# Kernel tuning notes

Measured on AMD Instinct MI355X. Metric: run time of the kernel, lower is better.

The kernel has to match this reference:

```python
import jax, jax.numpy as jnp
import numpy as np

B, N, D = 64, 100, 32            # batch, nodes, node feature size
FE = [96, 160, 192]              # edge-MLP layer sizes
FN = [256, 256, 32]              # node-MLP layer sizes
ALPHA = 0.2                      # leaky relu slope


def _lin_init(key, fan_in, fan_out):
    kw, kb = jax.random.split(key)
    bound = 1.0 / np.sqrt(fan_in)
    w = jax.random.uniform(kw, (fan_in, fan_out), jnp.float32, -bound, bound)
    b = jax.random.uniform(kb, (fan_out,), jnp.float32, -bound, bound)
    return w, b


def setup_inputs() -> dict:
    key = jax.random.key(0)
    ks = jax.random.split(key, 7)
    d = {"x": jax.random.normal(ks[0], (B, N, D), jnp.float32)}
    fe_sizes = [2 * D] + FE                    # edge MLP: in = concat(x_i, x_j)
    fn_sizes = [FE[-1] + D] + FN               # node MLP: in = concat(agg, x)
    for li in range(3):
        w, b = _lin_init(ks[1 + li], fe_sizes[li], fe_sizes[li + 1])
        d[f"fe_w{li}"], d[f"fe_b{li}"] = w, b
    for li in range(3):
        w, b = _lin_init(ks[4 + li], fn_sizes[li], fn_sizes[li + 1])
        d[f"fn_w{li}"], d[f"fn_b{li}"] = w, b
    return d


def reference(x, fe_w0, fe_b0, fe_w1, fe_b1, fe_w2, fe_b2,
              fn_w0, fn_b0, fn_w1, fn_b1, fn_w2, fn_b2):
    b, n, d = x.shape
    lr = lambda v: jax.nn.leaky_relu(v, ALPHA)
    # fully-connected pairwise edge features: A[b,i,j] = concat(x_i, x_j)
    xi = jnp.broadcast_to(x[:, :, None, :], (b, n, n, d))
    xj = jnp.broadcast_to(x[:, None, :, :], (b, n, n, d))
    a = jnp.concatenate([xi, xj], axis=-1)          # [b, n, n, 2d]
    # edge MLP (fe): leaky relu after every layer (final_linear=False)
    a = lr(a @ fe_w0 + fe_b0)
    a = lr(a @ fe_w1 + fe_b1)
    a = lr(a @ fe_w2 + fe_b2)                       # [b, n, n, FE[-1]]
    # sum aggregation over neighbors j
    agg = jnp.sum(a, axis=2)                        # [b, n, FE[-1]]
    # node MLP (fn): final layer linear (final_linear=True)
    h = jnp.concatenate([agg, x], axis=-1)          # [b, n, FE[-1]+d]
    h = lr(h @ fn_w0 + fn_b0)
    h = lr(h @ fn_w1 + fn_b1)
    h = h @ fn_w2 + fn_b2                           # [b, n, FN[-1]]
    return h
```

## Files before the change

kernel.cpp:

```cpp
#include <hip/hip_runtime.h>

#define B_    64
#define N_    100
#define D_    32
#define F0    96
#define F1    160
#define F2    192
#define HID   256
#define FOUT  32

typedef unsigned short u16;
typedef unsigned int   u32;
typedef u16   u16x8 __attribute__((ext_vector_type(8)));
typedef u32   u32x2 __attribute__((ext_vector_type(2)));
typedef __bf16 bf16x8 __attribute__((ext_vector_type(8)));
typedef float  fx4   __attribute__((ext_vector_type(4)));

__device__ __forceinline__ u16 f2bf(float f) {
    return __builtin_bit_cast(u16, (__bf16)f);
}
__device__ __forceinline__ float lrelu(float v) { return fmaxf(v, 0.2f * v); }

__device__ __forceinline__ bf16x8 fragLds(const u16* p) {
    return __builtin_bit_cast(bf16x8, *(const u16x8*)p);
}
__device__ __forceinline__ bf16x8 fragGbl(const u16* __restrict__ p) {
    return __builtin_bit_cast(bf16x8, *(const u16x8*)p);
}
#define MFMA(a, b, c) __builtin_amdgcn_mfma_f32_16x16x32_bf16((a), (b), (c), 0, 0, 0)

__device__ __forceinline__ u32x2 quadPack(u32 h) {
    u32 h1 = (u32)__shfl_xor((int)h, 1, 64);
    u32 pk = h | (h1 << 16);
    u32 pko = (u32)__shfl_xor((int)pk, 2, 64);
    return (u32x2){pk, pko};
}

#define OFF_P     0u
#define OFF_V     2457600u
#define OFF_AGG   4915200u
#define OFF_PACK  7372800u
#define PK_W1     0
#define PK_W2     15360
#define PK_N0     46080
#define PK_N1     103424
#define PK_N2     168960
#define PK_TOTAL  177152

#define PV_BLOCKS 2400
#define PACK_BLOCKS 346

__global__ __launch_bounds__(512) void prep_kernel(
    const float* __restrict__ x,
    const float* __restrict__ few0, const float* __restrict__ feb0,
    const float* __restrict__ few1, const float* __restrict__ few2,
    const float* __restrict__ fnw0, const float* __restrict__ fnw1,
    const float* __restrict__ fnw2,
    float* __restrict__ P, float* __restrict__ V, u16* __restrict__ wpack)
{
    const int blk = blockIdx.x, tid = threadIdx.x;
    if (blk < PV_BLOCKS) {
        int o = blk * 512 + tid;
        int r = o / 192, h = o - r * 192;
        const float* xr = x + r * D_;
        if (h < F0) {
            float acc = feb0[h];
            #pragma unroll
            for (int d = 0; d < D_; ++d) acc = fmaf(xr[d], few0[d * F0 + h], acc);
            P[r * F0 + h] = acc;
        } else {
            int k = h - F0;
            float acc = 0.f;
            #pragma unroll
            for (int d = 0; d < D_; ++d) acc = fmaf(xr[d], few0[(D_ + d) * F0 + k], acc);
            V[r * F0 + k] = acc;
        }
    } else {
        int p = (blk - PV_BLOCKS) * 512 + tid;
        const float* src; int start, Ncols, NT;
        if (p < PK_W2)      { start = PK_W1; src = few1; Ncols = F1;   NT = 10; }
        else if (p < PK_N0) { start = PK_W2; src = few2; Ncols = F2;   NT = 12; }
        else if (p < PK_N1) { start = PK_N0; src = fnw0; Ncols = HID;  NT = 16; }
        else if (p < PK_N2) { start = PK_N1; src = fnw1; Ncols = HID;  NT = 16; }
        else                { start = PK_N2; src = fnw2; Ncols = FOUT; NT = 2;  }
        int local = p - start;
        int j = local & 7, lane = (local >> 3) & 63, rest = local >> 9;
        int nt = rest % NT, kt = rest / NT;
        int n = 16 * nt + (lane & 15);
        int k = 32 * kt + 8 * (lane >> 4) + j;
        wpack[p] = f2bf(src[k * Ncols + n]);
    }
}

__global__ __launch_bounds__(512, 4) void edge_kernel(
    const float* __restrict__ P, const float* __restrict__ V,
    const u16* __restrict__ W1p, const u16* __restrict__ W2p,
    const float* __restrict__ feb1, const float* __restrict__ feb2,
    u16* __restrict__ agg)
{
    const int i = blockIdx.x, b = blockIdx.y;
    const int tid = threadIdx.x, ld = tid & 63, wv = tid >> 6;
    const int wn = wv & 3, wm = wv >> 2;
    const int row = b * N_ + i;

    __shared__ __align__(16) u16  sA0p[7 * 3 * 512];
    __shared__ __align__(16) u16  sA1p[7 * 5 * 512];
    __shared__ __align__(16) float sP[F0];
    __shared__ __align__(16) float sAggP[2 * F2];

    if (tid < F0) sP[tid] = P[row * F0 + tid];
    __syncthreads();

    {
        const float* Vb = V + b * N_ * F0;
        #pragma unroll
        for (int s = 0; s < 3; ++s) {
            int idx = tid + 512 * s;
            if (idx < 1344) {
                int lane = idx & 63, rest = idx >> 6;
                int kt = rest % 3, mt = rest / 3;
                int k = 32 * kt + 8 * (lane >> 4);
                int m = 16 * mt + (lane & 15);
                u16x8 w;
                if (m < N_) {
                    const float* vp = Vb + m * F0 + k;
                    fx4 v0 = *(const fx4*)(vp);
                    fx4 v1 = *(const fx4*)(vp + 4);
                    fx4 p0 = *(const fx4*)(sP + k);
                    fx4 p1 = *(const fx4*)(sP + k + 4);
                    #pragma unroll
                    for (int jj = 0; jj < 4; ++jj) {
                        w[jj]     = f2bf(lrelu(p0[jj] + v0[jj]));
                        w[4 + jj] = f2bf(lrelu(p1[jj] + v1[jj]));
                    }
                } else {
                    w = (u16x8){0, 0, 0, 0, 0, 0, 0, 0};
                }
                *(u16x8*)(sA0p + idx * 8) = w;
            }
        }
    }
    __syncthreads();

    const int mtB = wm ? 4 : 0, mtE = wm ? 7 : 4;
    const int c = ld & 15, rlo = (ld >> 4) * 4;
    const int a1off = (ld * 16) ^ (((ld >> 3) & 7) << 4);

    {
        const int nCnt = (wn < 2) ? 3 : 2;
        bf16x8 bw[3][3]; float bias[3];
        #pragma unroll
        for (int t = 0; t < 3; ++t) if (t < nCnt) {
            int nt = wn + 4 * t;
            bias[t] = feb1[16 * nt + c];
            #pragma unroll
            for (int kt = 0; kt < 3; ++kt)
                bw[t][kt] = fragGbl(W1p + (size_t)((kt * 10 + nt) * 64 + ld) * 8);
        }
        for (int mt = mtB; mt < mtE; ++mt) {
            bf16x8 a[3];
            #pragma unroll
            for (int kt = 0; kt < 3; ++kt)
                a[kt] = fragLds(sA0p + ((mt * 3 + kt) * 64 + ld) * 8);
            fx4 acc[3];
            #pragma unroll
            for (int t = 0; t < 3; ++t) acc[t] = (fx4){0.f, 0.f, 0.f, 0.f};
            #pragma unroll
            for (int kt = 0; kt < 3; ++kt)
                #pragma unroll
                for (int t = 0; t < 3; ++t)
                    if (t < nCnt) acc[t] = MFMA(a[kt], bw[t][kt], acc[t]);
            #pragma unroll
            for (int t = 0; t < 3; ++t) if (t < nCnt) {
                int nt = wn + 4 * t;
                int f = 16 * nt + c;
                int lq = (f >> 3) & 3;
                int S  = (((rlo >> 3) + 2 * lq) & 7) << 4;
                char* base = (char*)sA1p + (mt * 5 + (nt >> 1)) * 1024 + (c & 4) * 2;
                #pragma unroll
                for (int r = 0; r < 4; ++r) {
                    u32 h = (u32)f2bf(lrelu(acc[t][r] + bias[t]));
                    u32x2 two = quadPack(h);
                    int rowl = rlo + 16 * lq + r;
                    if ((ld & 3) == 0)
                        *(u32x2*)(base + ((rowl * 16) ^ S)) = two;
                }
            }
        }
    }
    __syncthreads();

    {
        bf16x8 bw[3][5]; float bias[3];
        float aggp[3] = {0.f, 0.f, 0.f};
        #pragma unroll
        for (int t = 0; t < 3; ++t) {
            int nt = wn + 4 * t;
            bias[t] = feb2[16 * nt + c];
            #pragma unroll
            for (int kt = 0; kt < 5; ++kt)
                bw[t][kt] = fragGbl(W2p + (size_t)((kt * 12 + nt) * 64 + ld) * 8);
        }
        for (int mt = mtB; mt < mtE; ++mt) {
            bf16x8 a[5];
            const char* rb = (const char*)sA1p + mt * 5120 + a1off;
            #pragma unroll
            for (int kt = 0; kt < 5; ++kt)
                a[kt] = fragLds((const u16*)(rb + kt * 1024));
            fx4 acc[3];
            #pragma unroll
            for (int t = 0; t < 3; ++t) acc[t] = (fx4){0.f, 0.f, 0.f, 0.f};
            #pragma unroll
            for (int kt = 0; kt < 5; ++kt)
                #pragma unroll
                for (int t = 0; t < 3; ++t)
                    acc[t] = MFMA(a[kt], bw[t][kt], acc[t]);
            bool ok = (mt < 6) || (rlo == 0);
            if (ok) {
                #pragma unroll
                for (int t = 0; t < 3; ++t)
                    #pragma unroll
                    for (int r = 0; r < 4; ++r)
                        aggp[t] += lrelu(acc[t][r] + bias[t]);
            }
        }
        #pragma unroll
        for (int t = 0; t < 3; ++t) {
            aggp[t] += __shfl_xor(aggp[t], 16, 64);
            aggp[t] += __shfl_xor(aggp[t], 32, 64);
        }
        if (ld < 16) {
            #pragma unroll
            for (int t = 0; t < 3; ++t)
                sAggP[wm * F2 + 16 * (wn + 4 * t) + ld] = aggp[t];
        }
    }
    __syncthreads();

    if (tid < F2) {
        float v = sAggP[tid] + sAggP[F2 + tid];
        agg[(size_t)row * F2 + tid] = f2bf(v);
    }
}

__global__ __launch_bounds__(512, 4) void node_kernel(
    const u16* __restrict__ agg, const float* __restrict__ x,
    const u16* __restrict__ n0p, const u16* __restrict__ n1p,
    const u16* __restrict__ n2p,
    const float* __restrict__ fnb0, const float* __restrict__ fnb1,
    const float* __restrict__ fnb2,
    float* __restrict__ out)
{
    const int blk = blockIdx.x;
    const int tid = threadIdx.x, ld = tid & 63, wv = tid >> 6;
    const int wn = wv & 3, mt = wv >> 2;
    const int c = ld & 15, rlo = (ld >> 4) * 4;
    const int c0 = c & ~3;

    __shared__ __align__(16) u16 sH0p[2 * 7 * 512];
    __shared__ __align__(16) u16 sH1p[2 * 8 * 512];
    __shared__ __align__(16) u16 sH2p[2 * 8 * 512];

    #pragma unroll
    for (int s = 0; s < 2; ++s) {
        int idx = tid + 512 * s;
        if (idx < 896) {
            int lane = idx & 63, rest = idx >> 6;
            int kt = rest % 7, mtt = rest / 7;
            int k = 32 * kt + 8 * (lane >> 4);
            int m = 16 * mtt + (lane & 15);
            int g = 32 * blk + m;
            u16x8 w;
            if (k < F2) {
                w = *(const u16x8*)(agg + (size_t)g * F2 + k);
            } else {
                const float* xp = x + (size_t)g * D_ + (k - F2);
                fx4 v0 = *(const fx4*)xp;
                fx4 v1 = *(const fx4*)(xp + 4);
                #pragma unroll
                for (int jj = 0; jj < 4; ++jj) {
                    w[jj] = f2bf(v0[jj]); w[4 + jj] = f2bf(v1[jj]);
                }
            }
            *(u16x8*)(sH0p + idx * 8) = w;
        }
    }
    __syncthreads();

    {
        fx4 acc[4];
        #pragma unroll
        for (int t = 0; t < 4; ++t) acc[t] = (fx4){0.f, 0.f, 0.f, 0.f};
        for (int kt = 0; kt < 7; ++kt) {
            bf16x8 a = fragLds(sH0p + ((mt * 7 + kt) * 64 + ld) * 8);
            #pragma unroll
            for (int t = 0; t < 4; ++t) {
                bf16x8 bw = fragGbl(n0p + (size_t)((kt * 16 + wn + 4 * t) * 64 + ld) * 8);
                acc[t] = MFMA(a, bw, acc[t]);
            }
        }
        #pragma unroll
        for (int t = 0; t < 4; ++t) {
            int f = 16 * (wn + 4 * t) + c;
            float bias = fnb0[f];
            int kt2 = f >> 5, lq = (f >> 3) & 3;
            u16* basep = sH1p + ((mt * 8 + kt2) * 64 + rlo + 16 * lq) * 8 + (c0 & 7);
            #pragma unroll
            for (int r = 0; r < 4; ++r) {
                u32 h = (u32)f2bf(lrelu(acc[t][r] + bias));
                u32x2 two = quadPack(h);
                if ((ld & 3) == 0)
                    *(u32x2*)(basep + r * 8) = two;
            }
        }
    }
    __syncthreads();

    {
        fx4 acc[4];
        #pragma unroll
        for (int t = 0; t < 4; ++t) acc[t] = (fx4){0.f, 0.f, 0.f, 0.f};
        for (int kt = 0; kt < 8; ++kt) {
            bf16x8 a = fragLds(sH1p + ((mt * 8 + kt) * 64 + ld) * 8);
            #pragma unroll
            for (int t = 0; t < 4; ++t) {
                bf16x8 bw = fragGbl(n1p + (size_t)((kt * 16 + wn + 4 * t) * 64 + ld) * 8);
                acc[t] = MFMA(a, bw, acc[t]);
            }
        }
        #pragma unroll
        for (int t = 0; t < 4; ++t) {
            int f = 16 * (wn + 4 * t) + c;
            float bias = fnb1[f];
            int kt2 = f >> 5, lq = (f >> 3) & 3;
            u16* basep = sH2p + ((mt * 8 + kt2) * 64 + rlo + 16 * lq) * 8 + (c0 & 7);
            #pragma unroll
            for (int r = 0; r < 4; ++r) {
                u32 h = (u32)f2bf(lrelu(acc[t][r] + bias));
                u32x2 two = quadPack(h);
                if ((ld & 3) == 0)
                    *(u32x2*)(basep + r * 8) = two;
            }
        }
    }
    __syncthreads();

    if (wv < 4) {
        int mt2 = wv >> 1, nt = wv & 1;
        fx4 acc = (fx4){0.f, 0.f, 0.f, 0.f};
        for (int kt = 0; kt < 8; ++kt) {
            bf16x8 a = fragLds(sH2p + ((mt2 * 8 + kt) * 64 + ld) * 8);
            bf16x8 bw = fragGbl(n2p + (size_t)((kt * 2 + nt) * 64 + ld) * 8);
            acc = MFMA(a, bw, acc);
        }
        int f = 16 * nt + c;
        float bias = fnb2[f];
        #pragma unroll
        for (int r = 0; r < 4; ++r) {
            int g = 32 * blk + 16 * mt2 + rlo + r;
            out[(size_t)g * FOUT + f] = acc[r] + bias;
        }
    }
}

extern "C" void kernel_launch(void* const* d_in, const int* in_sizes, int n_in,
                              void* d_out, int out_size, void* d_ws, size_t ws_size,
                              hipStream_t stream) {
    const float* x    = (const float*)d_in[0];
    const float* few0 = (const float*)d_in[1];
    const float* feb0 = (const float*)d_in[2];
    const float* few1 = (const float*)d_in[3];
    const float* feb1 = (const float*)d_in[4];
    const float* few2 = (const float*)d_in[5];
    const float* feb2 = (const float*)d_in[6];
    const float* fnw0 = (const float*)d_in[7];
    const float* fnb0 = (const float*)d_in[8];
    const float* fnw1 = (const float*)d_in[9];
    const float* fnb1 = (const float*)d_in[10];
    const float* fnw2 = (const float*)d_in[11];
    const float* fnb2 = (const float*)d_in[12];

    char* w = (char*)d_ws;
    float* P    = (float*)(w + OFF_P);
    float* V    = (float*)(w + OFF_V);
    u16*   aggb = (u16*)(w + OFF_AGG);
    u16*   pack = (u16*)(w + OFF_PACK);

    prep_kernel<<<PV_BLOCKS + PACK_BLOCKS, 512, 0, stream>>>(
        x, few0, feb0, few1, few2, fnw0, fnw1, fnw2, P, V, pack);

    edge_kernel<<<dim3(N_, B_), 512, 0, stream>>>(
        P, V, pack + PK_W1, pack + PK_W2, feb1, feb2, aggb);

    node_kernel<<<200, 512, 0, stream>>>(
        aggb, x, pack + PK_N0, pack + PK_N1, pack + PK_N2,
        fnb0, fnb1, fnb2, (float*)d_out);
}
```

Measured before the change: 245.8 us.

## Split edge kernel neighbor range across two blocks with atomic fp32 aggregation

Each (row, batch) edge block is split along the neighbor dimension into two blocks via a z grid dimension, each handling about half of the 7 neighbor tiles with smaller shared-memory buffers. Partial sums are combined with fp32 atomicAdd into a float aggregate buffer, which prep_kernel zeroes, and node_kernel converts to bf16 when loading. The aim is more parallelism and lower per-block LDS use, which should raise occupancy. In exchange the work per block is uneven (4 vs 3 tiles), the P/V setup and weight-fragment loads are repeated in both halves, and the atomics and larger fp32 intermediate add memory traffic.

```diff
diff --git a/kernel.cpp b/kernel.cpp
--- a/kernel.cpp
+++ b/kernel.cpp
@@ -39,7 +39,7 @@
 #define OFF_P     0u
 #define OFF_V     2457600u
 #define OFF_AGG   4915200u
-#define OFF_PACK  7372800u
+#define OFF_PACK  9830400u
 #define PK_W1     0
 #define PK_W2     15360
 #define PK_N0     46080
@@ -56,11 +56,13 @@
     const float* __restrict__ few1, const float* __restrict__ few2,
     const float* __restrict__ fnw0, const float* __restrict__ fnw1,
     const float* __restrict__ fnw2,
-    float* __restrict__ P, float* __restrict__ V, u16* __restrict__ wpack)
+    float* __restrict__ P, float* __restrict__ V, u16* __restrict__ wpack,
+    float* __restrict__ aggF)
 {
     const int blk = blockIdx.x, tid = threadIdx.x;
     if (blk < PV_BLOCKS) {
         int o = blk * 512 + tid;
+        aggF[o] = 0.f;
         int r = o / 192, h = o - r * 192;
         const float* xr = x + r * D_;
         if (h < F0) {
@@ -96,15 +98,17 @@
     const float* __restrict__ P, const float* __restrict__ V,
     const u16* __restrict__ W1p, const u16* __restrict__ W2p,
     const float* __restrict__ feb1, const float* __restrict__ feb2,
-    u16* __restrict__ agg)
+    float* __restrict__ aggF)
 {
-    const int i = blockIdx.x, b = blockIdx.y;
+    const int i = blockIdx.x, b = blockIdx.y, half = blockIdx.z;
     const int tid = threadIdx.x, ld = tid & 63, wv = tid >> 6;
     const int wn = wv & 3, wm = wv >> 2;
     const int row = b * N_ + i;
-
-    __shared__ __align__(16) u16  sA0p[7 * 3 * 512];
-    __shared__ __align__(16) u16  sA1p[7 * 5 * 512];
+    const int mt0 = half ? 4 : 0;
+    const int nSl = half ? 3 : 4;
+
+    __shared__ __align__(16) u16  sA0p[4 * 3 * 512];
+    __shared__ __align__(16) u16  sA1p[4 * 5 * 512];
     __shared__ __align__(16) float sP[F0];
     __shared__ __align__(16) float sAggP[2 * F2];
 
@@ -112,15 +116,16 @@
     __syncthreads();
 
     {
-        const float* Vb = V + b * N_ * F0;
-        #pragma unroll
-        for (int s = 0; s < 3; ++s) {
+        const float* Vb = V + (size_t)b * N_ * F0;
+        const int pairs = nSl * 3;
+        #pragma unroll
+        for (int s = 0; s < 2; ++s) {
             int idx = tid + 512 * s;
-            if (idx < 1344) {
+            if (idx < pairs * 64) {
                 int lane = idx & 63, rest = idx >> 6;
-                int kt = rest % 3, mt = rest / 3;
+                int kt = rest % 3, mtl = rest / 3;
                 int k = 32 * kt + 8 * (lane >> 4);
-                int m = 16 * mt + (lane & 15);
+                int m = 16 * (mt0 + mtl) + (lane & 15);
                 u16x8 w;
                 if (m < N_) {
                     const float* vp = Vb + m * F0 + k;
@@ -142,7 +147,8 @@
     }
     __syncthreads();
 
-    const int mtB = wm ? 4 : 0, mtE = wm ? 7 : 4;
+    const int mtb = mt0 + 2 * wm;
+    const int mte = half ? (wm ? 7 : 6) : (mtb + 2);
     const int c = ld & 15, rlo = (ld >> 4) * 4;
     const int a1off = (ld * 16) ^ (((ld >> 3) & 7) << 4);
 
@@ -157,11 +163,12 @@
             for (int kt = 0; kt < 3; ++kt)
                 bw[t][kt] = fragGbl(W1p + (size_t)((kt * 10 + nt) * 64 + ld) * 8);
         }
-        for (int mt = mtB; mt < mtE; ++mt) {
+        for (int mt = mtb; mt < mte; ++mt) {
+            int mtl = mt - mt0;
             bf16x8 a[3];
             #pragma unroll
             for (int kt = 0; kt < 3; ++kt)
-                a[kt] = fragLds(sA0p + ((mt * 3 + kt) * 64 + ld) * 8);
+                a[kt] = fragLds(sA0p + ((mtl * 3 + kt) * 64 + ld) * 8);
             fx4 acc[3];
             #pragma unroll
             for (int t = 0; t < 3; ++t) acc[t] = (fx4){0.f, 0.f, 0.f, 0.f};
@@ -176,7 +183,7 @@
                 int f = 16 * nt + c;
                 int lq = (f >> 3) & 3;
                 int S  = (((rlo >> 3) + 2 * lq) & 7) << 4;
-                char* base = (char*)sA1p + (mt * 5 + (nt >> 1)) * 1024 + (c & 4) * 2;
+                char* base = (char*)sA1p + ((mt & 3) * 5 + (nt >> 1)) * 1024 + (c & 4) * 2;
                 #pragma unroll
                 for (int r = 0; r < 4; ++r) {
                     u32 h = (u32)f2bf(lrelu(acc[t][r] + bias[t]));
@@ -201,9 +208,9 @@
             for (int kt = 0; kt < 5; ++kt)
                 bw[t][kt] = fragGbl(W2p + (size_t)((kt * 12 + nt) * 64 + ld) * 8);
         }
-        for (int mt = mtB; mt < mtE; ++mt) {
+        for (int mt = mtb; mt < mte; ++mt) {
             bf16x8 a[5];
-            const char* rb = (const char*)sA1p + mt * 5120 + a1off;
+            const char* rb = (const char*)sA1p + (mt & 3) * 5120 + a1off;
             #pragma unroll
             for (int kt = 0; kt < 5; ++kt)
                 a[kt] = fragLds((const u16*)(rb + kt * 1024));
@@ -239,12 +246,12 @@
 
     if (tid < F2) {
         float v = sAggP[tid] + sAggP[F2 + tid];
-        agg[(size_t)row * F2 + tid] = f2bf(v);
+        atomicAdd(aggF + (size_t)row * F2 + tid, v);
     }
 }
 
 __global__ __launch_bounds__(512, 4) void node_kernel(
-    const u16* __restrict__ agg, const float* __restrict__ x,
+    const float* __restrict__ aggF, const float* __restrict__ x,
     const u16* __restrict__ n0p, const u16* __restrict__ n1p,
     const u16* __restrict__ n2p,
     const float* __restrict__ fnb0, const float* __restrict__ fnb1,
@@ -272,7 +279,13 @@
             int g = 32 * blk + m;
             u16x8 w;
             if (k < F2) {
-                w = *(const u16x8*)(agg + (size_t)g * F2 + k);
+                const float* ap = aggF + (size_t)g * F2 + k;
+                fx4 a0 = *(const fx4*)ap;
+                fx4 a1 = *(const fx4*)(ap + 4);
+                #pragma unroll
+                for (int jj = 0; jj < 4; ++jj) {
+                    w[jj] = f2bf(a0[jj]); w[4 + jj] = f2bf(a1[jj]);
+                }
             } else {
                 const float* xp = x + (size_t)g * D_ + (k - F2);
                 fx4 v0 = *(const fx4*)xp;
@@ -383,16 +396,16 @@
     char* w = (char*)d_ws;
     float* P    = (float*)(w + OFF_P);
     float* V    = (float*)(w + OFF_V);
-    u16*   aggb = (u16*)(w + OFF_AGG);
+    float* aggF = (float*)(w + OFF_AGG);
     u16*   pack = (u16*)(w + OFF_PACK);
 
     prep_kernel<<<PV_BLOCKS + PACK_BLOCKS, 512, 0, stream>>>(
-        x, few0, feb0, few1, few2, fnw0, fnw1, fnw2, P, V, pack);
-
-    edge_kernel<<<dim3(N_, B_), 512, 0, stream>>>(
-        P, V, pack + PK_W1, pack + PK_W2, feb1, feb2, aggb);
+        x, few0, feb0, few1, few2, fnw0, fnw1, fnw2, P, V, pack, aggF);
+
+    edge_kernel<<<dim3(N_, B_, 2), 512, 0, stream>>>(
+        P, V, pack + PK_W1, pack + PK_W2, feb1, feb2, aggF);
 
     node_kernel<<<200, 512, 0, stream>>>(
-        aggb, x, pack + PK_N0, pack + PK_N1, pack + PK_N2,
+        aggF, x, pack + PK_N0, pack + PK_N1, pack + PK_N2,
         fnb0, fnb1, fnb2, (float*)d_out);
 }
```

New measurement: 279.9 us. 1.14x slower.
